# Kernel optimization log

Hardware: AMD Instinct MI355X
Metric: run time of the kernel (lower is better)

The kernel has to match this reference:

```python
import jax, jax.numpy as jnp
import numpy as np

N_CLASSES = 64
NUM_PROPAGATIONS = 3
TEMPERATURE = 1.0
IN_FEAT = 512
EMB_DIM = 128
N_SUPPORT = 3200
N_QUERY = 200000


def _cdist(a, b):
    # Euclidean distance [N, C] without materializing [N, C, D]
    a2 = jnp.sum(a * a, axis=-1, keepdims=True)          # [N, 1]
    b2 = jnp.sum(b * b, axis=-1)[None, :]                # [1, C]
    d2 = a2 + b2 - 2.0 * (a @ b.T)
    return jnp.sqrt(jnp.maximum(d2, 0.0))


def setup_inputs() -> dict:
    key = jax.random.key(0)
    k1, k2, k3, k4 = jax.random.split(key, 4)
    support = jax.random.normal(k1, (1, N_SUPPORT, IN_FEAT), dtype=jnp.float32)
    query = jax.random.normal(k2, (1, N_QUERY, IN_FEAT), dtype=jnp.float32)
    support_labels = (jnp.arange(N_SUPPORT, dtype=jnp.int32) % N_CLASSES)
    # encoder: Linear(IN_FEAT -> EMB_DIM)
    W = jax.random.normal(k3, (IN_FEAT, EMB_DIM), dtype=jnp.float32) * 0.05
    b = jax.random.normal(k4, (EMB_DIM,), dtype=jnp.float32) * 0.05
    return {"support": support, "query": query, "support_labels": support_labels,
            "W": W, "b": b}


def reference(support, query, support_labels, W, b):
    s_emb = support[0] @ W + b            # [Ns, D]
    q_emb = query[0] @ W + b              # [Nq, D]
    all_emb = jnp.concatenate([s_emb, q_emb], axis=0)   # [N, D]
    n_total = all_emb.shape[0]

    # initial prototypes: per-class mean of support embeddings (segment mean)
    sums = jax.ops.segment_sum(s_emb, support_labels, num_segments=N_CLASSES)
    counts = jax.ops.segment_sum(jnp.ones((s_emb.shape[0],), s_emb.dtype),
                                 support_labels, num_segments=N_CLASSES)
    prototypes = sums / jnp.maximum(counts, 1.0)[:, None]   # [C, D]

    attn = jax.nn.softmax(-_cdist(all_emb, prototypes) / TEMPERATURE, axis=-1)  # [N, C]
    for _ in range(NUM_PROPAGATIONS):
        # attention-weighted mean prototype: mean_n attn[n, c] * emb[n]
        prototypes = (attn.T @ all_emb) / n_total            # [C, D]
        attn = jax.nn.softmax(-_cdist(all_emb, prototypes) / TEMPERATURE, axis=-1)

    logits = -_cdist(q_emb, prototypes) / TEMPERATURE        # [Nq, C]
    return logits[None]                                      # [1, Nq, C]
```

## Files before the change

### kernel.cpp

```cpp
#include <hip/hip_runtime.h>

#define NS 3200
#define NQ 200000
#define NTOT (NS + NQ)
#define KIN 512
#define ED 128
#define NC 64
#define INV_N (1.0f / (float)NTOT)
#define PGRID 512

typedef short short8 __attribute__((ext_vector_type(8)));
typedef short short4v __attribute__((ext_vector_type(4)));
typedef float floatx4 __attribute__((ext_vector_type(4)));

static __device__ __forceinline__ unsigned short f2bf(float f) {
    unsigned int u = __float_as_uint(f);
    u += 0x7FFF + ((u >> 16) & 1);
    return (unsigned short)(u >> 16);
}
static __device__ __forceinline__ float bf2f(unsigned short h) {
    return __uint_as_float(((unsigned int)h) << 16);
}

__global__ __launch_bounds__(256) void prep_wt(const float* __restrict__ W,
                                               unsigned short* __restrict__ WT)
{
    int idx = blockIdx.x * 256 + threadIdx.x;
#pragma unroll
    for (int p = 0; p < 4; ++p) {
        int id = idx + p * 16384;
        int n = id >> 9, k = id & 511;
        WT[n * 512 + k] = f2bf(W[k * 128 + n]);
    }
}

__global__ __launch_bounds__(256) void encode_mfma(
    const float* __restrict__ X, const unsigned short* __restrict__ WT,
    const float* __restrict__ bias, unsigned short* __restrict__ emb,
    float* __restrict__ en2)
{
    __shared__ unsigned short Xs[2][64 * 72];

    const int t = threadIdx.x;
    const int w = t >> 6, lane = t & 63, q = lane >> 4, i = lane & 15;
    const long row0 = (long)blockIdx.x * 64;

    const int sr = t >> 4;
    const int skf = t & 15;
    const float* xbase = &X[(row0 + sr) * KIN + skf * 4];

    floatx4 acc[8];
#pragma unroll
    for (int ct = 0; ct < 8; ++ct) acc[ct] = (floatx4){0.f, 0.f, 0.f, 0.f};

    float4 L[4];
#define STAGE_LOAD(S)                                                          \
    {                                                                          \
        _Pragma("unroll")                                                      \
        for (int p = 0; p < 4; ++p)                                            \
            L[p] = *(const float4*)&xbase[(long)p * 16 * KIN + (S) * 64];      \
    }
#define STAGE_WRITE(B)                                                         \
    {                                                                          \
        _Pragma("unroll")                                                      \
        for (int p = 0; p < 4; ++p) {                                          \
            short4v h;                                                         \
            h[0] = (short)f2bf(L[p].x); h[1] = (short)f2bf(L[p].y);            \
            h[2] = (short)f2bf(L[p].z); h[3] = (short)f2bf(L[p].w);            \
            *(short4v*)&Xs[B][(sr + p * 16) * 72 + skf * 4] = h;               \
        }                                                                      \
    }

    STAGE_LOAD(0)
    STAGE_WRITE(0)

#pragma unroll
    for (int s = 0; s < 8; ++s) {
        if (s < 7) STAGE_LOAD(s + 1)
        __syncthreads();
        const unsigned short* xsb = &Xs[s & 1][0];
#pragma unroll
        for (int ks = 0; ks < 2; ++ks) {
            short8 a = *(const short8*)&xsb[(w * 16 + i) * 72 + ks * 32 + q * 8];
#pragma unroll
            for (int ct = 0; ct < 8; ++ct) {
                short8 b = *(const short8*)&WT[(ct * 16 + i) * 512 + s * 64 + ks * 32 + q * 8];
                acc[ct] = __builtin_amdgcn_mfma_f32_16x16x32_bf16(a, b, acc[ct], 0, 0, 0);
            }
        }
        if (s < 7) STAGE_WRITE((s + 1) & 1)
    }
#undef STAGE_LOAD
#undef STAGE_WRITE

    float sq[4] = {0.f, 0.f, 0.f, 0.f};
#pragma unroll
    for (int ct = 0; ct < 8; ++ct) {
        float bb = bias[ct * 16 + i];
#pragma unroll
        for (int r = 0; r < 4; ++r) {
            float v = acc[ct][r] + bb;
            long row = row0 + w * 16 + q * 4 + r;
            emb[row * ED + ct * 16 + i] = f2bf(v);
            sq[r] += v * v;
        }
    }
#pragma unroll
    for (int r = 0; r < 4; ++r) {
        float s = sq[r];
        s += __shfl_xor(s, 1); s += __shfl_xor(s, 2);
        s += __shfl_xor(s, 4); s += __shfl_xor(s, 8);
        if (i == 0) en2[row0 + w * 16 + q * 4 + r] = s;
    }
}

__global__ __launch_bounds__(128) void proto_init(
    const unsigned short* __restrict__ emb, const int* __restrict__ labels,
    float* __restrict__ proto)
{
    const int c = blockIdx.x, d = threadIdx.x;
    float acc = 0.f; int cnt = 0;
    for (int r4 = 0; r4 < NS; r4 += 4) {
        int4 lb = *(const int4*)&labels[r4];
        if (lb.x == c) { acc += bf2f(emb[(r4 + 0) * ED + d]); cnt++; }
        if (lb.y == c) { acc += bf2f(emb[(r4 + 1) * ED + d]); cnt++; }
        if (lb.z == c) { acc += bf2f(emb[(r4 + 2) * ED + d]); cnt++; }
        if (lb.w == c) { acc += bf2f(emb[(r4 + 3) * ED + d]); cnt++; }
    }
    proto[c * ED + d] = acc / fmaxf((float)cnt, 1.0f);
}

__global__ __launch_bounds__(256) void propagate(
    const unsigned short* __restrict__ emb, const float* __restrict__ en2,
    const float* __restrict__ proto_src, float scale,
    float* __restrict__ partial)
{
    __shared__ unsigned short Pbf[64 * 136];
    __shared__ unsigned short ET[128 * 66];
    __shared__ unsigned short ScT[64 * 72];
    __shared__ float pn2s[64];

    const int t = threadIdx.x;
    const int w = t >> 6, lane = t & 63, q = lane >> 4, i = lane & 15;

    {
        int c = t >> 2, part = t & 3;
        const float* src = &proto_src[c * 128 + part * 32];
        float sqv = 0.f;
#pragma unroll 8
        for (int j = 0; j < 32; ++j) {
            float v = src[j] * scale;
            Pbf[c * 136 + part * 32 + j] = f2bf(v);
            sqv += v * v;
        }
        sqv += __shfl_xor(sqv, 1);
        sqv += __shfl_xor(sqv, 2);
        if (part == 0) pn2s[c] = sqv;
    }
    __syncthreads();

    short8 bP[4][4];
#pragma unroll
    for (int ct = 0; ct < 4; ++ct)
#pragma unroll
        for (int ks = 0; ks < 4; ++ks)
            bP[ct][ks] = *(const short8*)&Pbf[(ct * 16 + i) * 136 + ks * 32 + q * 8];
    float pn[4];
#pragma unroll
    for (int ct = 0; ct < 4; ++ct) pn[ct] = pn2s[ct * 16 + i];

    floatx4 acc2[8];
#pragma unroll
    for (int nt = 0; nt < 8; ++nt) acc2[nt] = (floatx4){0.f, 0.f, 0.f, 0.f};

    const int ntiles = NTOT / 64;
    for (int tile = blockIdx.x; tile < ntiles; tile += gridDim.x) {
        const long row0 = (long)tile * 64;

        short8 aE[4];
#pragma unroll
        for (int ks = 0; ks < 4; ++ks)
            aE[ks] = *(const short8*)&emb[(row0 + w * 16 + i) * ED + ks * 32 + q * 8];
        float en[4];
#pragma unroll
        for (int r = 0; r < 4; ++r) en[r] = en2[row0 + w * 16 + q * 4 + r];

#pragma unroll
        for (int ks = 0; ks < 4; ++ks)
#pragma unroll
            for (int j = 0; j < 8; ++j)
                ET[(ks * 32 + q * 8 + j) * 66 + w * 16 + i] = (unsigned short)aE[ks][j];

        floatx4 s1[4];
#pragma unroll
        for (int ct = 0; ct < 4; ++ct) s1[ct] = (floatx4){0.f, 0.f, 0.f, 0.f};
#pragma unroll
        for (int ks = 0; ks < 4; ++ks)
#pragma unroll
            for (int ct = 0; ct < 4; ++ct)
                s1[ct] = __builtin_amdgcn_mfma_f32_16x16x32_bf16(aE[ks], bP[ct][ks], s1[ct], 0, 0, 0);

        float attn[4][4];
#pragma unroll
        for (int r = 0; r < 4; ++r) {
            float sc[4];
#pragma unroll
            for (int ct = 0; ct < 4; ++ct) {
                float d2 = en[r] + pn[ct] - 2.f * s1[ct][r];
                sc[ct] = -sqrtf(fmaxf(d2, 0.f));
            }
            float mx = fmaxf(fmaxf(sc[0], sc[1]), fmaxf(sc[2], sc[3]));
            mx = fmaxf(mx, __shfl_xor(mx, 1));
            mx = fmaxf(mx, __shfl_xor(mx, 2));
            mx = fmaxf(mx, __shfl_xor(mx, 4));
            mx = fmaxf(mx, __shfl_xor(mx, 8));
            float sm = 0.f;
#pragma unroll
            for (int ct = 0; ct < 4; ++ct) { attn[ct][r] = __expf(sc[ct] - mx); sm += attn[ct][r]; }
            sm += __shfl_xor(sm, 1);
            sm += __shfl_xor(sm, 2);
            sm += __shfl_xor(sm, 4);
            sm += __shfl_xor(sm, 8);
            float inv = 1.f / sm;
#pragma unroll
            for (int ct = 0; ct < 4; ++ct) attn[ct][r] *= inv;
        }
#pragma unroll
        for (int ct = 0; ct < 4; ++ct) {
            short4v pk;
            pk[0] = (short)f2bf(attn[ct][0]); pk[1] = (short)f2bf(attn[ct][1]);
            pk[2] = (short)f2bf(attn[ct][2]); pk[3] = (short)f2bf(attn[ct][3]);
            *(short4v*)&ScT[(ct * 16 + i) * 72 + w * 16 + q * 4] = pk;
        }
        __syncthreads();

#pragma unroll
        for (int ks2 = 0; ks2 < 2; ++ks2) {
            short8 a2 = *(const short8*)&ScT[(w * 16 + i) * 72 + ks2 * 32 + q * 8];
#pragma unroll
            for (int nt = 0; nt < 8; ++nt) {
                union { short8 s; unsigned int u[4]; } b2;
                const unsigned short* base = &ET[(nt * 16 + i) * 66 + ks2 * 32 + q * 8];
                b2.u[0] = *(const unsigned int*)&base[0];
                b2.u[1] = *(const unsigned int*)&base[2];
                b2.u[2] = *(const unsigned int*)&base[4];
                b2.u[3] = *(const unsigned int*)&base[6];
                acc2[nt] = __builtin_amdgcn_mfma_f32_16x16x32_bf16(a2, b2.s, acc2[nt], 0, 0, 0);
            }
        }
        __syncthreads();
    }

    float* myp = partial + (size_t)blockIdx.x * (NC * ED);
#pragma unroll
    for (int nt = 0; nt < 8; ++nt)
#pragma unroll
        for (int r = 0; r < 4; ++r)
            myp[(w * 16 + q * 4 + r) * ED + nt * 16 + i] = acc2[nt][r];
}

__global__ __launch_bounds__(256) void reduce_partials(
    const float* __restrict__ partial, float* __restrict__ proto)
{
    int idx = blockIdx.x * 256 + threadIdx.x;
    float s = 0.f;
#pragma unroll 8
    for (int b = 0; b < PGRID; ++b) s += partial[(size_t)b * (NC * ED) + idx];
    proto[idx] = s;
}

__global__ __launch_bounds__(256) void logits_k(
    const unsigned short* __restrict__ emb, const float* __restrict__ en2,
    const float* __restrict__ proto_src, float scale, float* __restrict__ out)
{
    __shared__ unsigned short Pbf[64 * 136];
    __shared__ float pn2s[64];

    const int t = threadIdx.x;
    const int w = t >> 6, lane = t & 63, q = lane >> 4, i = lane & 15;

    {
        int c = t >> 2, part = t & 3;
        const float* src = &proto_src[c * 128 + part * 32];
        float sqv = 0.f;
#pragma unroll 8
        for (int j = 0; j < 32; ++j) {
            float v = src[j] * scale;
            Pbf[c * 136 + part * 32 + j] = f2bf(v);
            sqv += v * v;
        }
        sqv += __shfl_xor(sqv, 1);
        sqv += __shfl_xor(sqv, 2);
        if (part == 0) pn2s[c] = sqv;
    }
    __syncthreads();

    short8 bP[4][4];
#pragma unroll
    for (int ct = 0; ct < 4; ++ct)
#pragma unroll
        for (int ks = 0; ks < 4; ++ks)
            bP[ct][ks] = *(const short8*)&Pbf[(ct * 16 + i) * 136 + ks * 32 + q * 8];
    float pn[4];
#pragma unroll
    for (int ct = 0; ct < 4; ++ct) pn[ct] = pn2s[ct * 16 + i];

    const int ntiles = NQ / 64;
    for (int tile = blockIdx.x; tile < ntiles; tile += gridDim.x) {
        const long row0 = (long)tile * 64;

        short8 aE[4];
#pragma unroll
        for (int ks = 0; ks < 4; ++ks)
            aE[ks] = *(const short8*)&emb[(row0 + w * 16 + i) * ED + ks * 32 + q * 8];
        float en[4];
#pragma unroll
        for (int r = 0; r < 4; ++r) en[r] = en2[row0 + w * 16 + q * 4 + r];

        floatx4 s1[4];
#pragma unroll
        for (int ct = 0; ct < 4; ++ct) s1[ct] = (floatx4){0.f, 0.f, 0.f, 0.f};
#pragma unroll
        for (int ks = 0; ks < 4; ++ks)
#pragma unroll
            for (int ct = 0; ct < 4; ++ct)
                s1[ct] = __builtin_amdgcn_mfma_f32_16x16x32_bf16(aE[ks], bP[ct][ks], s1[ct], 0, 0, 0);

#pragma unroll
        for (int r = 0; r < 4; ++r) {
            long row = row0 + w * 16 + q * 4 + r;
#pragma unroll
            for (int ct = 0; ct < 4; ++ct) {
                float d2 = en[r] + pn[ct] - 2.f * s1[ct][r];
                out[row * NC + ct * 16 + i] = -sqrtf(fmaxf(d2, 0.f));
            }
        }
    }
}

extern "C" void kernel_launch(void* const* d_in, const int* in_sizes, int n_in,
                              void* d_out, int out_size, void* d_ws, size_t ws_size,
                              hipStream_t stream)
{
    (void)in_sizes; (void)n_in; (void)out_size; (void)ws_size;

    const float* support = (const float*)d_in[0];
    const float* query   = (const float*)d_in[1];
    const int*   labels  = (const int*)d_in[2];
    const float* W       = (const float*)d_in[3];
    const float* bias    = (const float*)d_in[4];
    float* out = (float*)d_out;

    unsigned short* emb = (unsigned short*)d_ws;
    float* en2 = (float*)(emb + (size_t)NTOT * ED);
    unsigned short* WT = (unsigned short*)(en2 + NTOT);
    float* proto0 = (float*)(WT + 128 * 512);
    float* protoA = proto0 + NC * ED;
    float* protoB = protoA + NC * ED;
    float* part   = protoB + NC * ED;

    prep_wt<<<64, 256, 0, stream>>>(W, WT);
    encode_mfma<<<NS / 64, 256, 0, stream>>>(support, WT, bias, emb, en2);
    encode_mfma<<<NQ / 64, 256, 0, stream>>>(query, WT, bias,
                                             emb + (size_t)NS * ED, en2 + NS);
    proto_init<<<NC, ED, 0, stream>>>(emb, labels, proto0);

    propagate<<<PGRID, 256, 0, stream>>>(emb, en2, proto0, 1.0f, part);
    reduce_partials<<<32, 256, 0, stream>>>(part, protoA);

    propagate<<<PGRID, 256, 0, stream>>>(emb, en2, protoA, INV_N, part);
    reduce_partials<<<32, 256, 0, stream>>>(part, protoB);

    propagate<<<PGRID, 256, 0, stream>>>(emb, en2, protoB, INV_N, part);
    reduce_partials<<<32, 256, 0, stream>>>(part, protoA);

    logits_k<<<1024, 256, 0, stream>>>(emb + (size_t)NS * ED, en2 + NS,
                                       protoA, INV_N, out);
}
```

Measured before the change: 972.4 us.

## Use direct global-to-LDS loads in encoder, raise propagate grid, parallelize reductions

The encoder now stages fp32 input tiles straight into LDS with global_load_lds, using an XOR swizzle, and converts to bf16 only when building MFMA operands. The W fragments are also hoisted into registers per stage. The propagate kernel aliases its prototype and tile LDS buffers through a union to cut LDS use and allow more resident blocks, and runs on a larger grid. reduce_partials is split across many more blocks with an in-block tree over partial slices, and logits_k gets a larger grid. In exchange, the larger grid writes more partial buffers to memory, and the encoder LDS footprint doubles because tiles are kept in fp32.

```diff
diff --git a/kernel.cpp b/kernel.cpp
--- a/kernel.cpp
+++ b/kernel.cpp
@@ -7,7 +7,7 @@
 #define ED 128
 #define NC 64
 #define INV_N (1.0f / (float)NTOT)
-#define PGRID 512
+#define PGRID 1536
 
 typedef short short8 __attribute__((ext_vector_type(8)));
 typedef short short4v __attribute__((ext_vector_type(4)));
@@ -22,6 +22,12 @@
     return __uint_as_float(((unsigned int)h) << 16);
 }
 
+static __device__ __forceinline__ void gload_lds16(const float* g, float* l) {
+    __builtin_amdgcn_global_load_lds(
+        (const __attribute__((address_space(1))) void*)g,
+        (__attribute__((address_space(3))) void*)l, 16, 0, 0);
+}
+
 __global__ __launch_bounds__(256) void prep_wt(const float* __restrict__ W,
                                                unsigned short* __restrict__ WT)
 {
@@ -39,59 +45,62 @@
     const float* __restrict__ bias, unsigned short* __restrict__ emb,
     float* __restrict__ en2)
 {
-    __shared__ unsigned short Xs[2][64 * 72];
+    __shared__ float Xs[2][64 * 64];
 
     const int t = threadIdx.x;
     const int w = t >> 6, lane = t & 63, q = lane >> 4, i = lane & 15;
     const long row0 = (long)blockIdx.x * 64;
 
-    const int sr = t >> 4;
-    const int skf = t & 15;
-    const float* xbase = &X[(row0 + sr) * KIN + skf * 4];
+    const int srow = lane >> 4;
+    const int c4   = lane & 15;
 
     floatx4 acc[8];
 #pragma unroll
     for (int ct = 0; ct < 8; ++ct) acc[ct] = (floatx4){0.f, 0.f, 0.f, 0.f};
 
-    float4 L[4];
-#define STAGE_LOAD(S)                                                          \
-    {                                                                          \
-        _Pragma("unroll")                                                      \
-        for (int p = 0; p < 4; ++p)                                            \
-            L[p] = *(const float4*)&xbase[(long)p * 16 * KIN + (S) * 64];      \
-    }
-#define STAGE_WRITE(B)                                                         \
+#define STAGE(B, S)                                                            \
     {                                                                          \
         _Pragma("unroll")                                                      \
         for (int p = 0; p < 4; ++p) {                                          \
-            short4v h;                                                         \
-            h[0] = (short)f2bf(L[p].x); h[1] = (short)f2bf(L[p].y);            \
-            h[2] = (short)f2bf(L[p].z); h[3] = (short)f2bf(L[p].w);            \
-            *(short4v*)&Xs[B][(sr + p * 16) * 72 + skf * 4] = h;               \
+            int ii = w * 4 + p;                                                \
+            int r  = ii * 4 + srow;                                            \
+            int sw = (r & 7) << 2;                                             \
+            const float* g = &X[(row0 + r) * KIN + (S) * 64 + ((c4 * 4) ^ sw)];\
+            gload_lds16(g, &Xs[B][ii * 256]);                                  \
         }                                                                      \
     }
 
-    STAGE_LOAD(0)
-    STAGE_WRITE(0)
-
-#pragma unroll
+    STAGE(0, 0)
+
     for (int s = 0; s < 8; ++s) {
-        if (s < 7) STAGE_LOAD(s + 1)
         __syncthreads();
-        const unsigned short* xsb = &Xs[s & 1][0];
+        if (s < 7) STAGE((s + 1) & 1, s + 1)
+
+        short8 bfr[2][8];
+#pragma unroll
+        for (int ks = 0; ks < 2; ++ks)
+#pragma unroll
+            for (int ct = 0; ct < 8; ++ct)
+                bfr[ks][ct] = *(const short8*)&WT[(ct * 16 + i) * 512 + s * 64 + ks * 32 + q * 8];
+
+        const float* xb = &Xs[s & 1][(w * 16 + i) * 64];
+        const int swr = (i & 7) << 2;
 #pragma unroll
         for (int ks = 0; ks < 2; ++ks) {
-            short8 a = *(const short8*)&xsb[(w * 16 + i) * 72 + ks * 32 + q * 8];
-#pragma unroll
-            for (int ct = 0; ct < 8; ++ct) {
-                short8 b = *(const short8*)&WT[(ct * 16 + i) * 512 + s * 64 + ks * 32 + q * 8];
-                acc[ct] = __builtin_amdgcn_mfma_f32_16x16x32_bf16(a, b, acc[ct], 0, 0, 0);
-            }
-        }
-        if (s < 7) STAGE_WRITE((s + 1) & 1)
-    }
-#undef STAGE_LOAD
-#undef STAGE_WRITE
+            int c0 = ks * 32 + q * 8;
+            floatx4 fa = *(const floatx4*)&xb[c0 ^ swr];
+            floatx4 fb = *(const floatx4*)&xb[(c0 + 4) ^ swr];
+            short8 a;
+            a[0] = (short)f2bf(fa[0]); a[1] = (short)f2bf(fa[1]);
+            a[2] = (short)f2bf(fa[2]); a[3] = (short)f2bf(fa[3]);
+            a[4] = (short)f2bf(fb[0]); a[5] = (short)f2bf(fb[1]);
+            a[6] = (short)f2bf(fb[2]); a[7] = (short)f2bf(fb[3]);
+#pragma unroll
+            for (int ct = 0; ct < 8; ++ct)
+                acc[ct] = __builtin_amdgcn_mfma_f32_16x16x32_bf16(a, bfr[ks][ct], acc[ct], 0, 0, 0);
+        }
+    }
+#undef STAGE
 
     float sq[4] = {0.f, 0.f, 0.f, 0.f};
 #pragma unroll
@@ -135,9 +144,13 @@
     const float* __restrict__ proto_src, float scale,
     float* __restrict__ partial)
 {
-    __shared__ unsigned short Pbf[64 * 136];
-    __shared__ unsigned short ET[128 * 66];
-    __shared__ unsigned short ScT[64 * 72];
+    __shared__ union {
+        unsigned short Pbf[64 * 136];
+        struct {
+            unsigned short ET[128 * 66];
+            unsigned short ScT[64 * 72];
+        } m;
+    } sh;
     __shared__ float pn2s[64];
 
     const int t = threadIdx.x;
@@ -150,7 +163,7 @@
 #pragma unroll 8
         for (int j = 0; j < 32; ++j) {
             float v = src[j] * scale;
-            Pbf[c * 136 + part * 32 + j] = f2bf(v);
+            sh.Pbf[c * 136 + part * 32 + j] = f2bf(v);
             sqv += v * v;
         }
         sqv += __shfl_xor(sqv, 1);
@@ -164,10 +177,11 @@
     for (int ct = 0; ct < 4; ++ct)
 #pragma unroll
         for (int ks = 0; ks < 4; ++ks)
-            bP[ct][ks] = *(const short8*)&Pbf[(ct * 16 + i) * 136 + ks * 32 + q * 8];
+            bP[ct][ks] = *(const short8*)&sh.Pbf[(ct * 16 + i) * 136 + ks * 32 + q * 8];
     float pn[4];
 #pragma unroll
     for (int ct = 0; ct < 4; ++ct) pn[ct] = pn2s[ct * 16 + i];
+    __syncthreads();
 
     floatx4 acc2[8];
 #pragma unroll
@@ -189,7 +203,7 @@
         for (int ks = 0; ks < 4; ++ks)
 #pragma unroll
             for (int j = 0; j < 8; ++j)
-                ET[(ks * 32 + q * 8 + j) * 66 + w * 16 + i] = (unsigned short)aE[ks][j];
+                sh.m.ET[(ks * 32 + q * 8 + j) * 66 + w * 16 + i] = (unsigned short)aE[ks][j];
 
         floatx4 s1[4];
 #pragma unroll
@@ -230,17 +244,17 @@
             short4v pk;
             pk[0] = (short)f2bf(attn[ct][0]); pk[1] = (short)f2bf(attn[ct][1]);
             pk[2] = (short)f2bf(attn[ct][2]); pk[3] = (short)f2bf(attn[ct][3]);
-            *(short4v*)&ScT[(ct * 16 + i) * 72 + w * 16 + q * 4] = pk;
+            *(short4v*)&sh.m.ScT[(ct * 16 + i) * 72 + w * 16 + q * 4] = pk;
         }
         __syncthreads();
 
 #pragma unroll
         for (int ks2 = 0; ks2 < 2; ++ks2) {
-            short8 a2 = *(const short8*)&ScT[(w * 16 + i) * 72 + ks2 * 32 + q * 8];
+            short8 a2 = *(const short8*)&sh.m.ScT[(w * 16 + i) * 72 + ks2 * 32 + q * 8];
 #pragma unroll
             for (int nt = 0; nt < 8; ++nt) {
                 union { short8 s; unsigned int u[4]; } b2;
-                const unsigned short* base = &ET[(nt * 16 + i) * 66 + ks2 * 32 + q * 8];
+                const unsigned short* base = &sh.m.ET[(nt * 16 + i) * 66 + ks2 * 32 + q * 8];
                 b2.u[0] = *(const unsigned int*)&base[0];
                 b2.u[1] = *(const unsigned int*)&base[2];
                 b2.u[2] = *(const unsigned int*)&base[4];
@@ -262,11 +276,22 @@
 __global__ __launch_bounds__(256) void reduce_partials(
     const float* __restrict__ partial, float* __restrict__ proto)
 {
-    int idx = blockIdx.x * 256 + threadIdx.x;
+    __shared__ float red[256];
+    const int t = threadIdx.x;
+    const int o = blockIdx.x * 32 + (t & 31);
+    const int p = t >> 5;
     float s = 0.f;
-#pragma unroll 8
-    for (int b = 0; b < PGRID; ++b) s += partial[(size_t)b * (NC * ED) + idx];
-    proto[idx] = s;
+    const float* base = partial + (size_t)(p * (PGRID / 8)) * (NC * ED) + o;
+#pragma unroll 4
+    for (int b = 0; b < PGRID / 8; ++b) s += base[(size_t)b * (NC * ED)];
+    red[t] = s;
+    __syncthreads();
+    if (t < 32) {
+        float r = red[t];
+#pragma unroll
+        for (int pp = 1; pp < 8; ++pp) r += red[pp * 32 + t];
+        proto[o] = r;
+    }
 }
 
 __global__ __launch_bounds__(256) void logits_k(
@@ -366,14 +391,14 @@
     proto_init<<<NC, ED, 0, stream>>>(emb, labels, proto0);
 
     propagate<<<PGRID, 256, 0, stream>>>(emb, en2, proto0, 1.0f, part);
-    reduce_partials<<<32, 256, 0, stream>>>(part, protoA);
+    reduce_partials<<<256, 256, 0, stream>>>(part, protoA);
 
     propagate<<<PGRID, 256, 0, stream>>>(emb, en2, protoA, INV_N, part);
-    reduce_partials<<<32, 256, 0, stream>>>(part, protoB);
+    reduce_partials<<<256, 256, 0, stream>>>(part, protoB);
 
     propagate<<<PGRID, 256, 0, stream>>>(emb, en2, protoB, INV_N, part);
-    reduce_partials<<<32, 256, 0, stream>>>(part, protoA);
-
-    logits_k<<<1024, 256, 0, stream>>>(emb + (size_t)NS * ED, en2 + NS,
+    reduce_partials<<<256, 256, 0, stream>>>(part, protoA);
+
+    logits_k<<<2048, 256, 0, stream>>>(emb + (size_t)NS * ED, en2 + NS,
                                        protoA, INV_N, out);
 }
```

After: 963.3 us. No clear change (-0.9%).
